# Performance work log

Measured on AMD Instinct MI355X. Metric: run time of the kernel, lower is better.

The kernel has to match this reference:

```python
import jax, jax.numpy as jnp
import numpy as np

B_SZ, C_IN, C_OUT, H, W = 16, 32, 32, 128, 128
K, CODE, PAD, FACTOR = 3, 2, 1, 1.0

def setup_inputs() -> dict:
    key = jax.random.key(0)
    ks = jax.random.split(key, 7)
    s = 0.05
    return {
        "x": jax.random.normal(ks[0], (B_SZ, C_IN, H, W), jnp.float32),
        "codes": jax.random.normal(ks[1], (B_SZ, CODE, CODE), jnp.float32),
        "weight": jax.random.normal(ks[2], (C_OUT, C_IN, K, K), jnp.float32) * s,
        "A": jax.random.normal(ks[3], (C_IN, CODE, K, K), jnp.float32) * s,
        "Bm": jax.random.normal(ks[4], (C_OUT, CODE, K, K), jnp.float32) * s,
        "bias": jax.random.normal(ks[5], (C_OUT,), jnp.float32) * s,
        "bias_context": jax.random.normal(ks[6], (CODE, C_OUT), jnp.float32) * s,
    }

def reference(x, codes, weight, A, Bm, bias, bias_context):
    # hypernetwork weight synthesis: [b, out, in, k, k]
    w_ctx = jnp.einsum('ickl,bcr->birkl', A, codes)            # [b, in, code, k, k]
    w_ctx = jnp.einsum('birkl,orkl->boikl', w_ctx, Bm)         # [b, out, in, k, k]
    combined_weight = weight[None] + FACTOR * w_ctx
    # per-sample bias from diagonal of codes
    diag = jnp.diagonal(codes, axis1=-2, axis2=-1)             # [b, code]
    combined_bias = bias[None] + FACTOR * (diag @ bias_context)  # [b, out]
    # circular padding then per-sample VALID conv (== unfold + einsum)
    xp = jnp.pad(x, ((0, 0), (0, 0), (PAD, PAD), (PAD, PAD)), mode='wrap')
    def conv_one(xi, wi):
        return jax.lax.conv_general_dilated(
            xi[None], wi, window_strides=(1, 1), padding='VALID',
            dimension_numbers=('NCHW', 'OIHW', 'NCHW'))[0]
    out = jax.vmap(conv_one)(xp, combined_weight)              # [b, out, H, W]
    return out + combined_bias[:, :, None, None]
```

## Files before the change

kernel.cpp:

```cpp
#include <hip/hip_runtime.h>

typedef short bf16x8 __attribute__((ext_vector_type(8)));
typedef float f32x4  __attribute__((ext_vector_type(4)));
typedef unsigned int u32;

#define HH 128
#define WW 128

__device__ __forceinline__ u32 cvt_pk_bf16(float lo, float hi) {
    u32 r;
    asm volatile("v_cvt_pk_bf16_f32 %0, %1, %2" : "=v"(r) : "v"(lo), "v"(hi));
    return r;
}

__device__ __forceinline__ void lds_barrier() {
    asm volatile("s_waitcnt lgkmcnt(0)" ::: "memory");
    __builtin_amdgcn_s_barrier();
    __builtin_amdgcn_sched_barrier(0);
}

__global__ __launch_bounds__(512, 1) void geps_mfma_kernel(
    const float* __restrict__ x, const float* __restrict__ codes,
    const float* __restrict__ weight, const float* __restrict__ A,
    const float* __restrict__ Bm, const float* __restrict__ bias,
    const float* __restrict__ bctx, float* __restrict__ out)
{
    __shared__ bf16x8 lds_x[3072];
    __shared__ bf16x8 lds_w[1152];
    __shared__ float  lds_ctx[576];
    __shared__ float  lds_b[32];

    const int tid  = threadIdx.x;
    const int l    = tid & 63;
    const int wvid = tid >> 6;
    const int row  = wvid >> 2;
    const int nq   = wvid & 3;

    const int orig = blockIdx.x;
    const int vb   = (orig & 7) * 32 + (orig >> 3);
    const int b    = vb >> 4;
    const int grp  = vb & 15;
    const int h0   = grp * 8;

    const float c00 = codes[b * 4 + 0];
    const float c01 = codes[b * 4 + 1];
    const float c10 = codes[b * 4 + 2];
    const float c11 = codes[b * 4 + 3];

    for (int j = tid; j < 576; j += 512) {
        int i = j / 18, rem = j % 18, r = rem / 9, kl = rem % 9;
        float a0 = A[(i * 2 + 0) * 9 + kl];
        float a1 = A[(i * 2 + 1) * 9 + kl];
        lds_ctx[j] = (r == 0) ? (a0 * c00 + a1 * c10) : (a0 * c01 + a1 * c11);
    }
    if (tid < 32) lds_b[tid] = bias[tid] + c00 * bctx[tid] + c11 * bctx[32 + tid];
    lds_barrier();

    #pragma unroll
    for (int it = 0; it < 2; ++it) {
        int idx = it * 512 + tid;
        int cp  = idx & 63;
        int ig  = (idx >> 6) & 3;
        int rr  = idx >> 8;
        int c0  = cp * 2;
        int grow = (h0 - 1 + rr) & 127;
        const float* src = x + ((size_t)(b * 32 + ig * 8) * HH + grow) * WW + c0;
        float2 f[8];
        #pragma unroll
        for (int jj = 0; jj < 8; ++jj)
            f[jj] = *(const float2*)(src + (size_t)jj * HH * WW);
        u32 p0[4], p1[4];
        #pragma unroll
        for (int q = 0; q < 4; ++q) {
            p0[q] = cvt_pk_bf16(f[2 * q].x, f[2 * q + 1].x);
            p1[q] = cvt_pk_bf16(f[2 * q].y, f[2 * q + 1].y);
        }
        int didx = rr * 512 + (c0 >> 4) * 64 + ig * 16 + (c0 & 15);
        *(uint4*)&lds_x[didx]     = make_uint4(p0[0], p0[1], p0[2], p0[3]);
        *(uint4*)&lds_x[didx + 1] = make_uint4(p1[0], p1[1], p1[2], p1[3]);
    }

    for (int j = tid; j < 1152; j += 512) {
        int kl = j >> 7, rem = j & 127, o = rem >> 2, kb = rem & 3;
        float m0 = Bm[(o * 2 + 0) * 9 + kl];
        float m1 = Bm[(o * 2 + 1) * 9 + kl];
        float wf[8];
        #pragma unroll
        for (int jj = 0; jj < 8; ++jj) {
            int i = kb * 8 + jj;
            wf[jj] = weight[(o * 32 + i) * 9 + kl]
                   + lds_ctx[i * 18 + kl] * m0
                   + lds_ctx[i * 18 + 9 + kl] * m1;
        }
        u32 pk[4];
        #pragma unroll
        for (int q = 0; q < 4; ++q) pk[q] = cvt_pk_bf16(wf[2 * q], wf[2 * q + 1]);
        *(uint4*)&lds_w[kl * 128 + (o >> 4) * 64 + kb * 16 + (o & 15)] =
            make_uint4(pk[0], pk[1], pk[2], pk[3]);
    }
    lds_barrier();

    const int awb = (l >> 4) * 16 + (l & 15);
    bf16x8 af[9][2];
    #pragma unroll
    for (int kl = 0; kl < 9; ++kl)
        #pragma unroll
        for (int oh = 0; oh < 2; ++oh)
            af[kl][oh] = lds_w[kl * 128 + oh * 64 + awb];

    const int p = l & 15, igf = l >> 4;
    int bb[3];
    #pragma unroll
    for (int dl = -1; dl <= 1; ++dl) {
        int pq = p + dl;
        bb[dl + 1] = (pq & 15) + ((pq >> 4) << 6) + igf * 16;
    }

    float blr[2][4];
    #pragma unroll
    for (int oh = 0; oh < 2; ++oh)
        #pragma unroll
        for (int r = 0; r < 4; ++r)
            blr[oh][r] = lds_b[oh * 16 + (l >> 4) * 4 + r];

    const size_t obase0 = (size_t)(b * 32 + (l >> 4) * 4) * (HH * WW) + p;

    #pragma unroll
    for (int c = 0; c < 4; ++c) {
        float2 pf[8];
        int pcp = 0, pig = 0, prr = 0;
        if (c < 3) {
            int idx = tid;
            pcp = idx & 63;
            pig = (idx >> 6) & 3;
            prr = 4 + 2 * c + (idx >> 8);
            int grow = (h0 - 1 + prr) & 127;
            const float* src =
                x + ((size_t)(b * 32 + pig * 8) * HH + grow) * WW + pcp * 2;
            #pragma unroll
            for (int jj = 0; jj < 8; ++jj)
                pf[jj] = *(const float2*)(src + (size_t)jj * HH * WW);
        }

        f32x4 acc[2][2];
        #pragma unroll
        for (int oh = 0; oh < 2; ++oh)
            #pragma unroll
            for (int q = 0; q < 2; ++q) acc[oh][q] = (f32x4){0.f, 0.f, 0.f, 0.f};

        const int hr = 2 * c + row;
        #pragma unroll
        for (int lc = 0; lc < 3; ++lc) {
            #pragma unroll
            for (int k = 0; k < 3; ++k) {
                int s = hr + k; s = (s >= 6) ? s - 6 : s;
                const bf16x8 a0 = af[k * 3 + lc][0];
                const bf16x8 a1 = af[k * 3 + lc][1];
                #pragma unroll
                for (int q = 0; q < 2; ++q) {
                    int t = (bb[lc] + (nq * 2 + q) * 64) & 511;
                    bf16x8 bfv = lds_x[s * 512 + t];
                    acc[0][q] = __builtin_amdgcn_mfma_f32_16x16x32_bf16(
                        a0, bfv, acc[0][q], 0, 0, 0);
                    acc[1][q] = __builtin_amdgcn_mfma_f32_16x16x32_bf16(
                        a1, bfv, acc[1][q], 0, 0, 0);
                }
            }
        }

        const size_t ob = obase0 + (size_t)(h0 + hr) * WW;
        #pragma unroll
        for (int oh = 0; oh < 2; ++oh)
            #pragma unroll
            for (int q = 0; q < 2; ++q)
                #pragma unroll
                for (int r = 0; r < 4; ++r)
                    __builtin_nontemporal_store(
                        acc[oh][q][r] + blr[oh][r],
                        &out[ob + (size_t)(oh * 16 + r) * (HH * WW) +
                             (nq * 2 + q) * 16]);

        if (c < 3) {
            u32 p0[4], p1[4];
            #pragma unroll
            for (int q = 0; q < 4; ++q) {
                p0[q] = cvt_pk_bf16(pf[2 * q].x, pf[2 * q + 1].x);
                p1[q] = cvt_pk_bf16(pf[2 * q].y, pf[2 * q + 1].y);
            }
            int wslot = (prr >= 6) ? prr - 6 : prr;
            int c0 = pcp * 2;
            int didx = wslot * 512 + (c0 >> 4) * 64 + pig * 16 + (c0 & 15);
            *(uint4*)&lds_x[didx]     = make_uint4(p0[0], p0[1], p0[2], p0[3]);
            *(uint4*)&lds_x[didx + 1] = make_uint4(p1[0], p1[1], p1[2], p1[3]);
            lds_barrier();
        }
    }
}

extern "C" void kernel_launch(void* const* d_in, const int* in_sizes, int n_in,
                              void* d_out, int out_size, void* d_ws, size_t ws_size,
                              hipStream_t stream) {
    const float* x      = (const float*)d_in[0];
    const float* codes  = (const float*)d_in[1];
    const float* weight = (const float*)d_in[2];
    const float* A      = (const float*)d_in[3];
    const float* Bm     = (const float*)d_in[4];
    const float* bias   = (const float*)d_in[5];
    const float* bctx   = (const float*)d_in[6];
    float* out = (float*)d_out;

    hipLaunchKernelGGL(geps_mfma_kernel, dim3(256), dim3(512), 0, stream,
                       x, codes, weight, A, Bm, bias, bctx, out);
}
```

Measured before the change: 23.72 us.

## Split into bf16 pack kernel and direct-to-LDS conv kernel

Adds a pre-pass kernel that converts x to bf16 in the MFMA-friendly interleaved layout in workspace. The conv kernel then loads all ten needed input rows with global_load_lds DMA into a larger LDS buffer and computes a full output row per wave with 8 N-tiles, removing the rolling prefetch and in-loop barriers. It costs an extra kernel launch and an extra global round trip of the packed input, and it depends on workspace size, falling back to the old fused kernel otherwise.

Measured after the change: 30.46 us. 28.4% more time.

```diff
diff --git a/kernel.cpp b/kernel.cpp
--- a/kernel.cpp
+++ b/kernel.cpp
@@ -18,8 +18,165 @@
     __builtin_amdgcn_s_barrier();
     __builtin_amdgcn_sched_barrier(0);
 }
-
-__global__ __launch_bounds__(512, 1) void geps_mfma_kernel(
+__device__ __forceinline__ void full_barrier() {
+    asm volatile("s_waitcnt vmcnt(0) lgkmcnt(0)" ::: "memory");
+    __builtin_amdgcn_s_barrier();
+    __builtin_amdgcn_sched_barrier(0);
+}
+
+#define GLOBAL_LOAD_LDS16(g, l)                                              \
+    __builtin_amdgcn_global_load_lds(                                        \
+        (const __attribute__((address_space(1))) void*)(g),                  \
+        (__attribute__((address_space(3))) void*)(l), 16, 0, 0)
+
+__global__ __launch_bounds__(256) void geps_pack_kernel(
+    const float* __restrict__ x, u32* __restrict__ xb16)
+{
+    const int tid = threadIdx.x;
+    const int b   = blockIdx.x >> 7;
+    const int row = blockIdx.x & 127;
+    const int cp  = tid & 63;
+    const int ig  = tid >> 6;
+    const int c0  = cp * 2;
+
+    const float* src = x + ((size_t)(b * 32 + ig * 8) * HH + row) * WW + c0;
+    float2 f[8];
+    #pragma unroll
+    for (int jj = 0; jj < 8; ++jj)
+        f[jj] = *(const float2*)(src + (size_t)jj * HH * WW);
+    u32 p0[4], p1[4];
+    #pragma unroll
+    for (int q = 0; q < 4; ++q) {
+        p0[q] = cvt_pk_bf16(f[2 * q].x, f[2 * q + 1].x);
+        p1[q] = cvt_pk_bf16(f[2 * q].y, f[2 * q + 1].y);
+    }
+    int didx = (c0 >> 4) * 64 + ig * 16 + (c0 & 15);
+    u32* dst = xb16 + ((size_t)(b * 128 + row) * 512 + didx) * 4;
+    *(uint4*)&dst[0] = make_uint4(p0[0], p0[1], p0[2], p0[3]);
+    *(uint4*)&dst[4] = make_uint4(p1[0], p1[1], p1[2], p1[3]);
+}
+
+__global__ __launch_bounds__(512, 1) void geps_conv_kernel(
+    const u32* __restrict__ xb16, const float* __restrict__ codes,
+    const float* __restrict__ weight, const float* __restrict__ A,
+    const float* __restrict__ Bm, const float* __restrict__ bias,
+    const float* __restrict__ bctx, float* __restrict__ out)
+{
+    __shared__ bf16x8 lds_x[5120];
+    __shared__ bf16x8 lds_w[1152];
+    __shared__ float  lds_ctx[576];
+    __shared__ float  lds_b[32];
+
+    const int tid  = threadIdx.x;
+    const int l    = tid & 63;
+    const int row  = tid >> 6;
+
+    const int orig = blockIdx.x;
+    const int vb   = (orig & 7) * 32 + (orig >> 3);
+    const int b    = vb >> 4;
+    const int grp  = vb & 15;
+    const int h0   = grp * 8;
+
+    const char* xrow = (const char*)xb16 + (size_t)b * 128 * 8192;
+    #pragma unroll
+    for (int it = 0; it < 10; ++it) {
+        int grow = (h0 - 1 + it) & 127;
+        GLOBAL_LOAD_LDS16(xrow + (size_t)grow * 8192 + (size_t)tid * 16,
+                          (char*)lds_x + it * 8192 + tid * 16);
+    }
+
+    const float c00 = codes[b * 4 + 0];
+    const float c01 = codes[b * 4 + 1];
+    const float c10 = codes[b * 4 + 2];
+    const float c11 = codes[b * 4 + 3];
+    for (int j = tid; j < 576; j += 512) {
+        int i = j / 18, rem = j % 18, r = rem / 9, kl = rem % 9;
+        float a0 = A[(i * 2 + 0) * 9 + kl];
+        float a1 = A[(i * 2 + 1) * 9 + kl];
+        lds_ctx[j] = (r == 0) ? (a0 * c00 + a1 * c10) : (a0 * c01 + a1 * c11);
+    }
+    if (tid < 32) lds_b[tid] = bias[tid] + c00 * bctx[tid] + c11 * bctx[32 + tid];
+    lds_barrier();
+
+    for (int j = tid; j < 1152; j += 512) {
+        int kl = j >> 7, rem = j & 127, o = rem >> 2, kb = rem & 3;
+        float m0 = Bm[(o * 2 + 0) * 9 + kl];
+        float m1 = Bm[(o * 2 + 1) * 9 + kl];
+        float wf[8];
+        #pragma unroll
+        for (int jj = 0; jj < 8; ++jj) {
+            int i = kb * 8 + jj;
+            wf[jj] = weight[(o * 32 + i) * 9 + kl]
+                   + lds_ctx[i * 18 + kl] * m0
+                   + lds_ctx[i * 18 + 9 + kl] * m1;
+        }
+        u32 pk[4];
+        #pragma unroll
+        for (int q = 0; q < 4; ++q) pk[q] = cvt_pk_bf16(wf[2 * q], wf[2 * q + 1]);
+        *(uint4*)&lds_w[kl * 128 + (o >> 4) * 64 + kb * 16 + (o & 15)] =
+            make_uint4(pk[0], pk[1], pk[2], pk[3]);
+    }
+    full_barrier();
+
+    const int awb = (l >> 4) * 16 + (l & 15);
+    bf16x8 af[9][2];
+    #pragma unroll
+    for (int kl = 0; kl < 9; ++kl)
+        #pragma unroll
+        for (int oh = 0; oh < 2; ++oh)
+            af[kl][oh] = lds_w[kl * 128 + oh * 64 + awb];
+
+    const int p = l & 15, igf = l >> 4;
+    int bb[3];
+    #pragma unroll
+    for (int dl = -1; dl <= 1; ++dl) {
+        int pq = p + dl;
+        bb[dl + 1] = (pq & 15) + ((pq >> 4) << 6) + igf * 16;
+    }
+
+    f32x4 acc[2][8];
+    #pragma unroll
+    for (int oh = 0; oh < 2; ++oh)
+        #pragma unroll
+        for (int nt = 0; nt < 8; ++nt) acc[oh][nt] = (f32x4){0.f, 0.f, 0.f, 0.f};
+
+    #pragma unroll
+    for (int lc = 0; lc < 3; ++lc) {
+        #pragma unroll
+        for (int k = 0; k < 3; ++k) {
+            const bf16x8 a0 = af[k * 3 + lc][0];
+            const bf16x8 a1 = af[k * 3 + lc][1];
+            #pragma unroll
+            for (int nt = 0; nt < 8; ++nt) {
+                int t = (bb[lc] + nt * 64) & 511;
+                bf16x8 bfv = lds_x[(row + k) * 512 + t];
+                acc[0][nt] = __builtin_amdgcn_mfma_f32_16x16x32_bf16(
+                    a0, bfv, acc[0][nt], 0, 0, 0);
+                acc[1][nt] = __builtin_amdgcn_mfma_f32_16x16x32_bf16(
+                    a1, bfv, acc[1][nt], 0, 0, 0);
+            }
+        }
+    }
+
+    float blr[2][4];
+    #pragma unroll
+    for (int oh = 0; oh < 2; ++oh)
+        #pragma unroll
+        for (int r = 0; r < 4; ++r)
+            blr[oh][r] = lds_b[oh * 16 + (l >> 4) * 4 + r];
+
+    const size_t obase = ((size_t)(b * 32 + (l >> 4) * 4) * HH + h0 + row) * WW + p;
+    #pragma unroll
+    for (int oh = 0; oh < 2; ++oh)
+        #pragma unroll
+        for (int nt = 0; nt < 8; ++nt)
+            #pragma unroll
+            for (int r = 0; r < 4; ++r)
+                out[obase + (size_t)(oh * 16 + r) * (HH * WW) + nt * 16] =
+                    acc[oh][nt][r] + blr[oh][r];
+}
+
+__global__ __launch_bounds__(512, 1) void geps_mono_kernel(
     const float* __restrict__ x, const float* __restrict__ codes,
     const float* __restrict__ weight, const float* __restrict__ A,
     const float* __restrict__ Bm, const float* __restrict__ bias,
@@ -79,7 +236,6 @@
         *(uint4*)&lds_x[didx]     = make_uint4(p0[0], p0[1], p0[2], p0[3]);
         *(uint4*)&lds_x[didx + 1] = make_uint4(p1[0], p1[1], p1[2], p1[3]);
     }
-
     for (int j = tid; j < 1152; j += 512) {
         int kl = j >> 7, rem = j & 127, o = rem >> 2, kb = rem & 3;
         float m0 = Bm[(o * 2 + 0) * 9 + kl];
@@ -115,7 +271,6 @@
         int pq = p + dl;
         bb[dl + 1] = (pq & 15) + ((pq >> 4) << 6) + igf * 16;
     }
-
     float blr[2][4];
     #pragma unroll
     for (int oh = 0; oh < 2; ++oh)
@@ -141,13 +296,11 @@
             for (int jj = 0; jj < 8; ++jj)
                 pf[jj] = *(const float2*)(src + (size_t)jj * HH * WW);
         }
-
         f32x4 acc[2][2];
         #pragma unroll
         for (int oh = 0; oh < 2; ++oh)
             #pragma unroll
             for (int q = 0; q < 2; ++q) acc[oh][q] = (f32x4){0.f, 0.f, 0.f, 0.f};
-
         const int hr = 2 * c + row;
         #pragma unroll
         for (int lc = 0; lc < 3; ++lc) {
@@ -167,7 +320,6 @@
                 }
             }
         }
-
         const size_t ob = obase0 + (size_t)(h0 + hr) * WW;
         #pragma unroll
         for (int oh = 0; oh < 2; ++oh)
@@ -179,7 +331,6 @@
                         acc[oh][q][r] + blr[oh][r],
                         &out[ob + (size_t)(oh * 16 + r) * (HH * WW) +
                              (nq * 2 + q) * 16]);
-
         if (c < 3) {
             u32 p0[4], p1[4];
             #pragma unroll
@@ -209,6 +360,15 @@
     const float* bctx   = (const float*)d_in[6];
     float* out = (float*)d_out;
 
-    hipLaunchKernelGGL(geps_mfma_kernel, dim3(256), dim3(512), 0, stream,
-                       x, codes, weight, A, Bm, bias, bctx, out);
-}
+    const size_t need = (size_t)16 * 128 * 512 * 16;
+    if (ws_size >= need) {
+        u32* xb16 = (u32*)d_ws;
+        hipLaunchKernelGGL(geps_pack_kernel, dim3(2048), dim3(256), 0, stream,
+                           x, xb16);
+        hipLaunchKernelGGL(geps_conv_kernel, dim3(256), dim3(512), 0, stream,
+                           xb16, codes, weight, A, Bm, bias, bctx, out);
+    } else {
+        hipLaunchKernelGGL(geps_mono_kernel, dim3(256), dim3(512), 0, stream,
+                           x, codes, weight, A, Bm, bias, bctx, out);
+    }
+}
```
